# Kernel tuning notes

Hardware: AMD Instinct MI355X
Metric: run time of the kernel (lower is better)

The kernel has to match this reference:

```python
import jax, jax.numpy as jnp
import numpy as np

THRESHOLD = 8.0
BN_EPS = 1e-5


def setup_inputs() -> dict:
    key = jax.random.key(0)
    k1, k2 = jax.random.split(key)
    B, C, H, W = 2, 128, 64, 64
    x = jax.random.normal(k1, (B, C, H, W), dtype=jnp.float32)
    W_fc = jax.random.normal(k2, (C, C), dtype=jnp.float32) * (1.0 / np.sqrt(C))
    b_fc = jnp.zeros((C,), dtype=jnp.float32)
    gamma = jnp.ones((C,), dtype=jnp.float32)
    beta = jnp.zeros((C,), dtype=jnp.float32)
    return {"x": x, "W_fc": W_fc, "b_fc": b_fc, "gamma": gamma, "beta": beta}


def _mean_agg(X, path):
    # X: [B,N,C], path: [B,N,N] (col->row). out = rownorm(path) @ X
    out = jnp.matmul(path, X)
    s = jnp.sum(path, axis=2, keepdims=True)  # [B,N,1]
    norm = jnp.where(s > 0, 1.0 / s, 0.0)     # inf -> 0 as in torch code
    return norm * out


def reference(x, W_fc, b_fc, gamma, beta):
    b, c, h, w = x.shape
    N = h * w
    # [B,N,C] token features
    xf = jnp.transpose(x.reshape(b, c, N), (0, 2, 1))
    # pairwise euclidean distance (cdist, p=2)
    sq = jnp.sum(xf * xf, axis=-1)  # [B,N]
    d2 = sq[:, :, None] + sq[:, None, :] - 2.0 * jnp.einsum('bnc,bmc->bnm', xf, xf)
    dist = jnp.sqrt(jnp.maximum(d2, 0.0))
    Hg = (dist < THRESHOLD).astype(xf.dtype)  # [B,N,N] hypergraph incidence
    # HyperGraphConv: y = fc(x); E = mean(H^T @ y); out = mean(H @ E); res = y + out
    y = jnp.einsum('bnc,dc->bnd', xf, W_fc) + b_fc
    E = _mean_agg(y, jnp.swapaxes(Hg, 1, 2))
    x_out = _mean_agg(E, Hg)
    xe = y + x_out  # [B,N,C]
    # back to [B,C,H,W]
    xo = jnp.transpose(xe, (0, 2, 1)).reshape(b, c, h, w)
    # BatchNorm2d (training mode: batch stats over B,H,W) + SiLU
    mean = jnp.mean(xo, axis=(0, 2, 3), keepdims=True)
    var = jnp.var(xo, axis=(0, 2, 3), keepdims=True)
    xn = (xo - mean) * jax.lax.rsqrt(var + BN_EPS)
    xn = gamma[None, :, None, None] * xn + beta[None, :, None, None]
    return xn * jax.nn.sigmoid(xn)
```

## Files before the change

kernel.cpp:

```cpp
#include <hip/hip_runtime.h>

typedef unsigned short ushort_t;
typedef unsigned int   uint32;
typedef unsigned long long u64;
typedef __bf16 bf16_t;
typedef bf16_t bf16x8 __attribute__((ext_vector_type(8)));
typedef float  f32x4  __attribute__((ext_vector_type(4)));

#define N_TOK 4096
#define C_DIM 128
#define NTOT  8192
#define THRESH2 64.0f

#define XF_OFF  (0u)
#define YF_OFF  (2u<<20)
#define XE_OFF  (10u<<20)
#define SQ_OFF  (14u<<20)
#define BN_OFF  ((14u<<20) + 32768u)
#define HB_OFF  (16u<<20)
#define WS_NEED ((size_t)(24u<<20))

__device__ __forceinline__ ushort_t f2b(float f){
    uint32 u = __float_as_uint(f);
    u += 0x7fffu + ((u>>16)&1u);
    return (ushort_t)(u>>16);
}
__device__ __forceinline__ u64 shfl_u64(u64 v, int src){
    uint32 lo = (uint32)v, hi = (uint32)(v>>32);
    lo = __shfl(lo, src); hi = __shfl(hi, src);
    return ((u64)hi<<32)|lo;
}
__device__ __forceinline__ u64 shfl_xor_u64(u64 v, int m){
    uint32 lo = (uint32)v, hi = (uint32)(v>>32);
    lo = __shfl_xor(lo, m); hi = __shfl_xor(hi, m);
    return ((u64)hi<<32)|lo;
}
__device__ __forceinline__ int wave_popc_reduce(u64 w){
    int cnt = __builtin_popcountll(w);
    cnt += __shfl_xor(cnt, 1);
    cnt += __shfl_xor(cnt, 2);
    cnt += __shfl_xor(cnt, 4);
    cnt += __shfl_xor(cnt, 8);
    cnt += __shfl_xor(cnt, 16);
    cnt += __shfl_xor(cnt, 32);
    return cnt;
}

__global__ __launch_bounds__(256) void k_fc(const float* __restrict__ x,
                                            const float* __restrict__ W,
                                            const float* __restrict__ bfc,
                                            ushort_t* __restrict__ Xf,
                                            float* __restrict__ Yf,
                                            float* __restrict__ sq,
                                            float* __restrict__ bnp){
    __shared__ ushort_t Xs[64*136];
    __shared__ ushort_t Ws[64*136];
    int tid = threadIdx.x;
    int t0 = blockIdx.x * 64;
    int dh = blockIdx.y;
    int b  = t0 >> 12;
    int n0 = t0 & 4095;
    if (blockIdx.x == 0 && dh == 0){
        #pragma unroll
        for (int k=0;k<8;k++) bnp[tid + 256*k] = 0.f;
    }
    const float* xb = x + (size_t)b * C_DIM * N_TOK + n0;
    #pragma unroll
    for (int k=0;k<8;k++){
        int idx = tid + 256*k;
        int c = idx >> 4, n4 = (idx & 15)*4;
        float4 v = *(const float4*)(xb + (size_t)c*N_TOK + n4);
        Xs[(n4+0)*136 + c] = f2b(v.x);
        Xs[(n4+1)*136 + c] = f2b(v.y);
        Xs[(n4+2)*136 + c] = f2b(v.z);
        Xs[(n4+3)*136 + c] = f2b(v.w);
    }
    const float* Wb = W + (size_t)dh*64*C_DIM;
    #pragma unroll
    for (int k=0;k<8;k++){
        int idx = tid + 256*k;
        int d = idx >> 5, c4 = (idx & 31)*4;
        float4 v = *(const float4*)(Wb + d*C_DIM + c4);
        uint2 u;
        u.x = (uint32)f2b(v.x) | ((uint32)f2b(v.y)<<16);
        u.y = (uint32)f2b(v.z) | ((uint32)f2b(v.w)<<16);
        *(uint2*)(&Ws[d*136 + c4]) = u;
    }
    __syncthreads();
    #pragma unroll
    for (int k=0;k<2;k++){
        int idx = tid + 256*(k + 2*dh);
        int row = idx >> 4, c8 = (idx & 15)*8;
        uint4 o = *(const uint4*)(&Xs[row*136 + c8]);
        *(uint4*)(Xf + (size_t)(t0 + row)*C_DIM + c8) = o;
    }
    if (dh == 0){
        int tok = tid >> 2, p = tid & 3;
        const ushort_t* xr = &Xs[tok*136 + p*32];
        float sacc = 0.f;
        #pragma unroll
        for (int i=0;i<16;i++){
            uint32 u = *(const uint32*)(&xr[i*2]);
            float v0 = __uint_as_float(u<<16);
            float v1 = __uint_as_float(u & 0xffff0000u);
            sacc = fmaf(v0, v0, sacc);
            sacc = fmaf(v1, v1, sacc);
        }
        sacc += __shfl_xor(sacc, 1);
        sacc += __shfl_xor(sacc, 2);
        if (p == 0) sq[t0 + tok] = sacc;
    }
    int wv = tid >> 6, lane = tid & 63;
    int qd = lane >> 4, m = lane & 15;
    f32x4 acc[4] = {{0,0,0,0},{0,0,0,0},{0,0,0,0},{0,0,0,0}};
    #pragma unroll
    for (int kc=0;kc<4;kc++){
        bf16x8 af = *(const bf16x8*)(&Xs[(wv*16 + m)*136 + kc*32 + qd*8]);
        #pragma unroll
        for (int ct=0;ct<4;ct++){
            bf16x8 bfr = *(const bf16x8*)(&Ws[(ct*16+m)*136 + kc*32 + qd*8]);
            acc[ct] = __builtin_amdgcn_mfma_f32_16x16x32_bf16(af, bfr, acc[ct], 0, 0, 0);
        }
    }
    int row = t0 + wv*16 + qd*4;
    #pragma unroll
    for (int ct=0;ct<4;ct++){
        int d = dh*64 + ct*16 + m;
        float bias = bfc[d];
        #pragma unroll
        for (int r=0;r<4;r++)
            Yf[(size_t)(row + r)*C_DIM + d] = acc[ct][r] + bias;
    }
}

__global__ __launch_bounds__(256) void k_gram(const ushort_t* __restrict__ Xf,
                                              const float* __restrict__ sq,
                                              u64* __restrict__ Hb){
    __shared__ ushort_t Al[128*128];
    __shared__ ushort_t Bl[64*128];
    __shared__ u64 rowW[128];
    __shared__ u64 part[256];
    int tid = threadIdx.x;
    int L = blockIdx.x, b = blockIdx.y;
    int bi = (int)((65.0f - sqrtf(4225.0f - 4.0f*(float)L)) * 0.5f);
    while (bi > 0 && bi*(65-bi) > L) --bi;
    while ((bi+1)*(65-(bi+1)) <= L) ++bi;
    int bj = L - bi*(65-bi) + 2*bi;
    int i0 = bi*128, j0 = bj*64;
    const ushort_t* XfA = Xf + (size_t)(b*N_TOK + i0)*C_DIM;
    const ushort_t* XfB = Xf + (size_t)(b*N_TOK + j0)*C_DIM;
    #pragma unroll
    for (int k=0;k<8;k++){
        int q = tid + 256*k;
        int row = q >> 4, c16 = q & 15;
        int off = row*256 + ((c16*16) ^ ((row & 7) << 4));
        *(uint4*)((char*)Al + off) = *(const uint4*)(XfA + row*C_DIM + c16*8);
    }
    #pragma unroll
    for (int k=0;k<4;k++){
        int q = tid + 256*k;
        int row = q >> 4, c16 = q & 15;
        int off = row*256 + ((c16*16) ^ ((row & 7) << 4));
        *(uint4*)((char*)Bl + off) = *(const uint4*)(XfB + row*C_DIM + c16*8);
    }
    __syncthreads();
    int wv = tid >> 6, lane = tid & 63;
    int qd = lane >> 4, m = lane & 15;
    f32x4 acc[2][4] = {{{0,0,0,0},{0,0,0,0},{0,0,0,0},{0,0,0,0}},
                       {{0,0,0,0},{0,0,0,0},{0,0,0,0},{0,0,0,0}}};
    #pragma unroll
    for (int kc=0;kc<4;kc++){
        int coff = (kc*64 + qd*16) ^ ((m & 7) << 4);
        bf16x8 a0 = *(const bf16x8*)((char*)Al + (wv*32 +      m)*256 + coff);
        bf16x8 a1 = *(const bf16x8*)((char*)Al + (wv*32 + 16 + m)*256 + coff);
        #pragma unroll
        for (int ct=0;ct<4;ct++){
            bf16x8 bfr = *(const bf16x8*)((char*)Bl + (ct*16 + m)*256 + coff);
            acc[0][ct] = __builtin_amdgcn_mfma_f32_16x16x32_bf16(a0, bfr, acc[0][ct], 0, 0, 0);
            acc[1][ct] = __builtin_amdgcn_mfma_f32_16x16x32_bf16(a1, bfr, acc[1][ct], 0, 0, 0);
        }
    }
    float sqj[4];
    #pragma unroll
    for (int ct=0;ct<4;ct++) sqj[ct] = sq[b*N_TOK + j0 + ct*16 + m];
    #pragma unroll
    for (int rt=0;rt<2;rt++){
        int lr = wv*32 + rt*16 + qd*4;
        int ib = i0 + lr;
        float sqi[4];
        #pragma unroll
        for (int r=0;r<4;r++) sqi[r] = sq[b*N_TOK + ib + r];
        #pragma unroll
        for (int r=0;r<4;r++){
            u64 bits = 0;
            #pragma unroll
            for (int ct=0;ct<4;ct++){
                float d2 = sqi[r] + sqj[ct] - 2.0f*acc[rt][ct][r];
                if (d2 < THRESH2) bits |= (u64)1 << (ct*16 + m);
            }
            bits |= shfl_xor_u64(bits, 1);
            bits |= shfl_xor_u64(bits, 2);
            bits |= shfl_xor_u64(bits, 4);
            bits |= shfl_xor_u64(bits, 8);
            if (m == 0){
                Hb[(size_t)(b*N_TOK + ib + r)*64 + bj] = bits;
                rowW[lr + r] = bits;
            }
        }
    }
    __syncthreads();
    {
        int jj = tid & 63, hw = (tid>>6)&1, sub = tid>>7;
        u64 p = 0;
        int ibase = hw*64 + sub*32;
        #pragma unroll 8
        for (int ii=0; ii<32; ii++){
            u64 wrd = rowW[ibase + ii];
            p |= ((wrd >> jj) & 1ull) << (sub*32 + ii);
        }
        part[tid] = p;
    }
    __syncthreads();
    if (tid < 128){
        int jj = tid & 63, hw = tid >> 6;
        u64 wt = part[tid] | part[tid + 128];
        Hb[(size_t)(b*N_TOK + j0 + jj)*64 + 2*bi + hw] = wt;
    }
}

__global__ __launch_bounds__(256) void k_agg2(const u64* __restrict__ Hb,
                                              const float* __restrict__ Yf,
                                              float* __restrict__ Xe,
                                              float* __restrict__ bnp){
    __shared__ float r1[4][128];
    __shared__ float r2[4][128];
    int tid = threadIdx.x;
    int wv = tid >> 6, lane = tid & 63;
    int row = blockIdx.x * 4 + wv;
    int b = row >> 12;
    const float* Vb = Yf + (size_t)b*N_TOK*C_DIM;
    u64 myw = Hb[(size_t)row*64 + lane];
    int cnt = wave_popc_reduce(myw);
    float nrm_i = (cnt > 0) ? 1.0f/(float)cnt : 0.0f;
    float acc0 = 0.f, acc1 = 0.f;
    u64 nz = __ballot(myw != 0);
    while (nz){
        int wdi = __builtin_ctzll(nz);
        nz &= nz - 1;
        u64 mw = shfl_u64(myw, wdi);
        while (mw){
            int j = wdi*64 + __builtin_ctzll(mw);
            mw &= mw - 1;
            int jrow = (b << 12) + j;
            u64 jw; float nrm_j;
            if (jrow == row){
                jw = myw; nrm_j = nrm_i;
            } else {
                jw = Hb[(size_t)jrow*64 + lane];
                int jc = wave_popc_reduce(jw);
                nrm_j = (jc > 0) ? 1.0f/(float)jc : 0.0f;
            }
            float sub0 = 0.f, sub1 = 0.f;
            u64 jnz = __ballot(jw != 0);
            while (jnz){
                int w2 = __builtin_ctzll(jnz);
                jnz &= jnz - 1;
                u64 m2 = shfl_u64(jw, w2);
                while (m2){
                    int kk = w2*64 + __builtin_ctzll(m2);
                    m2 &= m2 - 1;
                    sub0 += Vb[(size_t)kk*C_DIM + lane];
                    sub1 += Vb[(size_t)kk*C_DIM + lane + 64];
                }
            }
            acc0 += nrm_j * sub0;
            acc1 += nrm_j * sub1;
        }
    }
    size_t o = (size_t)row*C_DIM;
    float xe0 = Yf[o + lane]      + nrm_i*acc0;
    float xe1 = Yf[o + lane + 64] + nrm_i*acc1;
    Xe[o + lane]      = xe0;
    Xe[o + lane + 64] = xe1;
    r1[wv][lane]      = xe0;
    r1[wv][lane + 64] = xe1;
    r2[wv][lane]      = xe0*xe0;
    r2[wv][lane + 64] = xe1*xe1;
    __syncthreads();
    if (tid < 128){
        float s1 = r1[0][tid]+r1[1][tid]+r1[2][tid]+r1[3][tid];
        float s2 = r2[0][tid]+r2[1][tid]+r2[2][tid]+r2[3][tid];
        int prt = blockIdx.x & 7;
        atomicAdd(&bnp[prt*256 + tid],       s1);
        atomicAdd(&bnp[prt*256 + 128 + tid], s2);
    }
}

__global__ __launch_bounds__(256) void k_out(const float* __restrict__ Xe,
                                             const float* __restrict__ bnp,
                                             const float* __restrict__ gamma,
                                             const float* __restrict__ beta,
                                             float* __restrict__ out){
    __shared__ float tile[32][33];
    int tx = threadIdx.x, ty = threadIdx.y;
    int n0 = blockIdx.x*32, c0 = blockIdx.y*32, b = blockIdx.z;
    int c = c0 + tx;
    float s1 = 0.f, s2 = 0.f;
    #pragma unroll
    for (int p=0;p<8;p++){
        s1 += bnp[p*256 + c];
        s2 += bnp[p*256 + 128 + c];
    }
    float inv = 1.0f / (float)NTOT;
    float mean = s1 * inv;
    float var  = s2*inv - mean*mean;
    float scale = gamma[c] * rsqrtf(var + 1e-5f);
    float shift = beta[c] - mean*scale;
    #pragma unroll
    for (int k=0;k<4;k++){
        int nl = ty + 8*k;
        float v = Xe[(size_t)(b*N_TOK + n0 + nl)*C_DIM + c];
        v = scale*v + shift;
        float sg = 1.0f/(1.0f + __expf(-v));
        tile[tx][nl] = v * sg;
    }
    __syncthreads();
    #pragma unroll
    for (int k=0;k<4;k++){
        int cl = ty + 8*k;
        out[(size_t)(b*C_DIM + c0 + cl)*N_TOK + n0 + tx] = tile[cl][tx];
    }
}

extern "C" void kernel_launch(void* const* d_in, const int* in_sizes, int n_in,
                              void* d_out, int out_size, void* d_ws, size_t ws_size,
                              hipStream_t stream){
    if (ws_size < WS_NEED) return;
    const float* x     = (const float*)d_in[0];
    const float* W     = (const float*)d_in[1];
    const float* bfc   = (const float*)d_in[2];
    const float* gamma = (const float*)d_in[3];
    const float* beta  = (const float*)d_in[4];
    char* ws = (char*)d_ws;
    ushort_t* Xf = (ushort_t*)(ws + XF_OFF);
    float*    Yf = (float*)(ws + YF_OFF);
    float*    Xe = (float*)(ws + XE_OFF);
    float*    sqp= (float*)(ws + SQ_OFF);
    float*    bnp= (float*)(ws + BN_OFF);
    u64*      Hb = (u64*)(ws + HB_OFF);
    float*    outp = (float*)d_out;

    k_fc  <<<dim3(128,2),  dim3(256),  0, stream>>>(x, W, bfc, Xf, Yf, sqp, bnp);
    k_gram<<<dim3(1056,2), dim3(256),  0, stream>>>(Xf, sqp, Hb);
    k_agg2<<<dim3(2048),   dim3(256),  0, stream>>>(Hb, Yf, Xe, bnp);
    k_out <<<dim3(128,4,2),dim3(32,8), 0, stream>>>(Xe, bnp, gamma, beta, outp);
}
```

Baseline: 102.6 us.

## Fuse aggregation and BatchNorm-SiLU output via grid-wide barrier

```diff
diff --git a/kernel.cpp b/kernel.cpp
--- a/kernel.cpp
+++ b/kernel.cpp
@@ -11,12 +11,13 @@
 #define C_DIM 128
 #define NTOT  8192
 #define THRESH2 64.0f
+#define AGG_BLOCKS 1024
 
 #define XF_OFF  (0u)
 #define YF_OFF  (2u<<20)
-#define XE_OFF  (10u<<20)
 #define SQ_OFF  (14u<<20)
 #define BN_OFF  ((14u<<20) + 32768u)
+#define CNT_OFF (BN_OFF + 8192u)
 #define HB_OFF  (16u<<20)
 #define WS_NEED ((size_t)(24u<<20))
 
@@ -52,7 +53,8 @@
                                             ushort_t* __restrict__ Xf,
                                             float* __restrict__ Yf,
                                             float* __restrict__ sq,
-                                            float* __restrict__ bnp){
+                                            float* __restrict__ bnp,
+                                            uint32* __restrict__ cnt){
     __shared__ ushort_t Xs[64*136];
     __shared__ ushort_t Ws[64*136];
     int tid = threadIdx.x;
@@ -63,6 +65,7 @@
     if (blockIdx.x == 0 && dh == 0){
         #pragma unroll
         for (int k=0;k<8;k++) bnp[tid + 256*k] = 0.f;
+        if (tid == 0) *cnt = 0u;
     }
     const float* xb = x + (size_t)b * C_DIM * N_TOK + n0;
     #pragma unroll
@@ -228,64 +231,74 @@
     }
 }
 
-__global__ __launch_bounds__(256) void k_agg2(const u64* __restrict__ Hb,
-                                              const float* __restrict__ Yf,
-                                              float* __restrict__ Xe,
-                                              float* __restrict__ bnp){
+__global__ __launch_bounds__(256, 4) void k_agg_out(const u64* __restrict__ Hb,
+                                                    const float* __restrict__ Yf,
+                                                    float* __restrict__ bnp,
+                                                    uint32* __restrict__ cnt,
+                                                    const float* __restrict__ gamma,
+                                                    const float* __restrict__ beta,
+                                                    float* __restrict__ out){
     __shared__ float r1[4][128];
     __shared__ float r2[4][128];
+    __shared__ float tile[128*9];
     int tid = threadIdx.x;
     int wv = tid >> 6, lane = tid & 63;
-    int row = blockIdx.x * 4 + wv;
-    int b = row >> 12;
+    int row0 = blockIdx.x * 8;
+    int b = row0 >> 12;
     const float* Vb = Yf + (size_t)b*N_TOK*C_DIM;
-    u64 myw = Hb[(size_t)row*64 + lane];
-    int cnt = wave_popc_reduce(myw);
-    float nrm_i = (cnt > 0) ? 1.0f/(float)cnt : 0.0f;
-    float acc0 = 0.f, acc1 = 0.f;
-    u64 nz = __ballot(myw != 0);
-    while (nz){
-        int wdi = __builtin_ctzll(nz);
-        nz &= nz - 1;
-        u64 mw = shfl_u64(myw, wdi);
-        while (mw){
-            int j = wdi*64 + __builtin_ctzll(mw);
-            mw &= mw - 1;
-            int jrow = (b << 12) + j;
-            u64 jw; float nrm_j;
-            if (jrow == row){
-                jw = myw; nrm_j = nrm_i;
-            } else {
-                jw = Hb[(size_t)jrow*64 + lane];
-                int jc = wave_popc_reduce(jw);
-                nrm_j = (jc > 0) ? 1.0f/(float)jc : 0.0f;
+    float xe0a, xe1a, xe0b, xe1b;
+    float s1a=0.f, s1b=0.f, s2a=0.f, s2b=0.f;
+    #pragma unroll
+    for (int k=0;k<2;k++){
+        int row = row0 + wv + 4*k;
+        u64 myw = Hb[(size_t)row*64 + lane];
+        int ci = wave_popc_reduce(myw);
+        float nrm_i = (ci > 0) ? 1.0f/(float)ci : 0.0f;
+        float acc0 = 0.f, acc1 = 0.f;
+        u64 nz = __ballot(myw != 0);
+        while (nz){
+            int wdi = __builtin_ctzll(nz);
+            nz &= nz - 1;
+            u64 mw = shfl_u64(myw, wdi);
+            while (mw){
+                int j = wdi*64 + __builtin_ctzll(mw);
+                mw &= mw - 1;
+                int jrow = (b << 12) + j;
+                u64 jw; float nrm_j;
+                if (jrow == row){ jw = myw; nrm_j = nrm_i; }
+                else {
+                    jw = Hb[(size_t)jrow*64 + lane];
+                    int jc = wave_popc_reduce(jw);
+                    nrm_j = (jc > 0) ? 1.0f/(float)jc : 0.0f;
+                }
+                float sub0 = 0.f, sub1 = 0.f;
+                u64 jnz = __ballot(jw != 0);
+                while (jnz){
+                    int w2 = __builtin_ctzll(jnz);
+                    jnz &= jnz - 1;
+                    u64 m2 = shfl_u64(jw, w2);
+                    while (m2){
+                        int kk = w2*64 + __builtin_ctzll(m2);
+                        m2 &= m2 - 1;
+                        sub0 += Vb[(size_t)kk*C_DIM + lane];
+                        sub1 += Vb[(size_t)kk*C_DIM + lane + 64];
+                    }
+                }
+                acc0 += nrm_j * sub0;
+                acc1 += nrm_j * sub1;
             }
-            float sub0 = 0.f, sub1 = 0.f;
-            u64 jnz = __ballot(jw != 0);
-            while (jnz){
-                int w2 = __builtin_ctzll(jnz);
-                jnz &= jnz - 1;
-                u64 m2 = shfl_u64(jw, w2);
-                while (m2){
-                    int kk = w2*64 + __builtin_ctzll(m2);
-                    m2 &= m2 - 1;
-                    sub0 += Vb[(size_t)kk*C_DIM + lane];
-                    sub1 += Vb[(size_t)kk*C_DIM + lane + 64];
-                }
-            }
-            acc0 += nrm_j * sub0;
-            acc1 += nrm_j * sub1;
-        }
-    }
-    size_t o = (size_t)row*C_DIM;
-    float xe0 = Yf[o + lane]      + nrm_i*acc0;
-    float xe1 = Yf[o + lane + 64] + nrm_i*acc1;
-    Xe[o + lane]      = xe0;
-    Xe[o + lane + 64] = xe1;
-    r1[wv][lane]      = xe0;
-    r1[wv][lane + 64] = xe1;
-    r2[wv][lane]      = xe0*xe0;
-    r2[wv][lane + 64] = xe1*xe1;
+        }
+        size_t o = (size_t)row*C_DIM;
+        float v0 = Yf[o + lane]      + nrm_i*acc0;
+        float v1 = Yf[o + lane + 64] + nrm_i*acc1;
+        if (k == 0){ xe0a = v0; xe1a = v1; } else { xe0b = v0; xe1b = v1; }
+        s1a += v0; s2a += v0*v0;
+        s1b += v1; s2b += v1*v1;
+    }
+    r1[wv][lane]      = s1a;
+    r1[wv][lane + 64] = s1b;
+    r2[wv][lane]      = s2a;
+    r2[wv][lane + 64] = s2b;
     __syncthreads();
     if (tid < 128){
         float s1 = r1[0][tid]+r1[1][tid]+r1[2][tid]+r1[3][tid];
@@ -294,41 +307,55 @@
         atomicAdd(&bnp[prt*256 + tid],       s1);
         atomicAdd(&bnp[prt*256 + 128 + tid], s2);
     }
-}
-
-__global__ __launch_bounds__(256) void k_out(const float* __restrict__ Xe,
-                                             const float* __restrict__ bnp,
-                                             const float* __restrict__ gamma,
-                                             const float* __restrict__ beta,
-                                             float* __restrict__ out){
-    __shared__ float tile[32][33];
-    int tx = threadIdx.x, ty = threadIdx.y;
-    int n0 = blockIdx.x*32, c0 = blockIdx.y*32, b = blockIdx.z;
-    int c = c0 + tx;
-    float s1 = 0.f, s2 = 0.f;
-    #pragma unroll
-    for (int p=0;p<8;p++){
-        s1 += bnp[p*256 + c];
-        s2 += bnp[p*256 + 128 + c];
-    }
+    __threadfence();
+    __syncthreads();
+    if (tid == 0){
+        __hip_atomic_fetch_add(cnt, 1u, __ATOMIC_RELEASE, __HIP_MEMORY_SCOPE_AGENT);
+        while (__hip_atomic_fetch_add(cnt, 0u, __ATOMIC_ACQUIRE, __HIP_MEMORY_SCOPE_AGENT)
+               < (uint32)AGG_BLOCKS)
+            __builtin_amdgcn_s_sleep(2);
+    }
+    __syncthreads();
     float inv = 1.0f / (float)NTOT;
-    float mean = s1 * inv;
-    float var  = s2*inv - mean*mean;
-    float scale = gamma[c] * rsqrtf(var + 1e-5f);
-    float shift = beta[c] - mean*scale;
-    #pragma unroll
-    for (int k=0;k<4;k++){
-        int nl = ty + 8*k;
-        float v = Xe[(size_t)(b*N_TOK + n0 + nl)*C_DIM + c];
-        v = scale*v + shift;
-        float sg = 1.0f/(1.0f + __expf(-v));
-        tile[tx][nl] = v * sg;
-    }
-    __syncthreads();
-    #pragma unroll
-    for (int k=0;k<4;k++){
-        int cl = ty + 8*k;
-        out[(size_t)(b*C_DIM + c0 + cl)*N_TOK + n0 + tx] = tile[cl][tx];
+    float scl_l, sft_l, scl_h, sft_h;
+    {
+        int cl = lane, ch = lane + 64;
+        float a1=0.f,a2=0.f,b1=0.f,b2=0.f;
+        #pragma unroll
+        for (int p=0;p<8;p++){
+            a1 += __hip_atomic_load(&bnp[p*256 + cl],       __ATOMIC_RELAXED, __HIP_MEMORY_SCOPE_AGENT);
+            a2 += __hip_atomic_load(&bnp[p*256 + 128 + cl], __ATOMIC_RELAXED, __HIP_MEMORY_SCOPE_AGENT);
+            b1 += __hip_atomic_load(&bnp[p*256 + ch],       __ATOMIC_RELAXED, __HIP_MEMORY_SCOPE_AGENT);
+            b2 += __hip_atomic_load(&bnp[p*256 + 128 + ch], __ATOMIC_RELAXED, __HIP_MEMORY_SCOPE_AGENT);
+        }
+        float mean = a1*inv, var = a2*inv - mean*mean;
+        scl_l = gamma[cl] * rsqrtf(var + 1e-5f);
+        sft_l = beta[cl] - mean*scl_l;
+        mean = b1*inv; var = b2*inv - mean*mean;
+        scl_h = gamma[ch] * rsqrtf(var + 1e-5f);
+        sft_h = beta[ch] - mean*scl_h;
+    }
+    #pragma unroll
+    for (int k=0;k<2;k++){
+        float v0 = (k==0) ? xe0a : xe0b;
+        float v1 = (k==0) ? xe1a : xe1b;
+        v0 = scl_l*v0 + sft_l;
+        v1 = scl_h*v1 + sft_h;
+        v0 = v0 / (1.0f + __expf(-v0));
+        v1 = v1 / (1.0f + __expf(-v1));
+        int n = wv + 4*k;
+        tile[lane*9 + n]       = v0;
+        tile[(lane+64)*9 + n]  = v1;
+    }
+    __syncthreads();
+    {
+        int c = tid >> 1, n4 = (tid & 1)*4;
+        float4 v;
+        v.x = tile[c*9 + n4 + 0];
+        v.y = tile[c*9 + n4 + 1];
+        v.z = tile[c*9 + n4 + 2];
+        v.w = tile[c*9 + n4 + 3];
+        *(float4*)(out + (size_t)(b*C_DIM + c)*N_TOK + (row0 & 4095) + n4) = v;
     }
 }
 
@@ -344,14 +371,13 @@
     char* ws = (char*)d_ws;
     ushort_t* Xf = (ushort_t*)(ws + XF_OFF);
     float*    Yf = (float*)(ws + YF_OFF);
-    float*    Xe = (float*)(ws + XE_OFF);
     float*    sqp= (float*)(ws + SQ_OFF);
     float*    bnp= (float*)(ws + BN_OFF);
+    uint32*   cnt= (uint32*)(ws + CNT_OFF);
     u64*      Hb = (u64*)(ws + HB_OFF);
     float*    outp = (float*)d_out;
 
-    k_fc  <<<dim3(128,2),  dim3(256),  0, stream>>>(x, W, bfc, Xf, Yf, sqp, bnp);
-    k_gram<<<dim3(1056,2), dim3(256),  0, stream>>>(Xf, sqp, Hb);
-    k_agg2<<<dim3(2048),   dim3(256),  0, stream>>>(Hb, Yf, Xe, bnp);
-    k_out <<<dim3(128,4,2),dim3(32,8), 0, stream>>>(Xe, bnp, gamma, beta, outp);
-}
+    k_fc     <<<dim3(128,2),    dim3(256), 0, stream>>>(x, W, bfc, Xf, Yf, sqp, bnp, cnt);
+    k_gram   <<<dim3(1056,2),   dim3(256), 0, stream>>>(Xf, sqp, Hb);
+    k_agg_out<<<dim3(AGG_BLOCKS),dim3(256),0, stream>>>(Hb, Yf, bnp, cnt, gamma, beta, outp);
+}
```

Measured after the change: 212.1 us. 107% more time.
